# Kernel tuning notes

Hardware: AMD Instinct MI355X
Metric: run time of the kernel (lower is better)

Reference implementation:

```python
import jax, jax.numpy as jnp
import numpy as np


def _hilbert_filter(S):
    # scipy.signal.hilbert analytic-signal spectrum multiplier
    h = np.zeros(S, dtype=np.float32)
    h[0] = 1.0
    if S % 2 == 0:
        h[S // 2] = 1.0
        h[1:S // 2] = 2.0
    else:
        h[1:(S + 1) // 2] = 2.0
    return h


def setup_inputs() -> dict:
    key = jax.random.key(0)
    B, C, S = 16, 64, 2048
    x = jax.random.normal(key, (B, C, S), dtype=jnp.float32)
    return {"x": x}


def reference(x) -> jnp.ndarray:
    B, C, S = x.shape
    h = jnp.asarray(_hilbert_filter(S))
    # Analytic signal via FFT (batched over all B*C channels at once,
    # instead of recomputing hilbert() per (i,j) pair as the torch loop does)
    analytic = jnp.fft.ifft(jnp.fft.fft(x, axis=-1) * h, axis=-1)  # [B,C,S] complex
    theta = jnp.angle(analytic)                                    # [B,C,S]
    # Pairwise instantaneous phase differences: [B,C,C,S]
    d = theta[:, :, None, :] - theta[:, None, :, :]
    # angle(exp(1j*d)) wraps d to (-pi,pi]; original zeroes exact +/-pi values.
    # sign(sin(d)) == sign(wrapped d) with +/-pi (and 0) mapped to 0 -- identical math.
    pli = jnp.abs(jnp.mean(jnp.sign(jnp.sin(d)), axis=-1))         # [B,C,C]
    # diagonal: d == 0 -> sign 0 -> mean 0, matching the skipped i==j entries
    return pli.astype(jnp.float32)
```

## Files before the change

### kernel.cpp

```cpp
#include <hip/hip_runtime.h>

#define Bv 16
#define Cv 64
#define Sv 2048
#define NSEG 64
#define SSEG 32
#define ROWS 68

__device__ __forceinline__ void bf_f(float2& u, float2& v, const float2 w) {
    const float dr = u.x - v.x, di = u.y - v.y;
    u.x += v.x; u.y += v.y;
    v.x = dr * w.x - di * w.y;
    v.y = dr * w.y + di * w.x;
}
__device__ __forceinline__ void bf_i(float2& u, float2& v, const float2 w) {
    const float vr = v.x * w.x + v.y * w.y;
    const float vi = v.y * w.x - v.x * w.y;
    v.x = u.x - vr; v.y = u.y - vi;
    u.x += vr; u.y += vi;
}
__device__ __forceinline__ float2 csq(const float2 a) {
    return make_float2(a.x * a.x - a.y * a.y, 2.0f * a.x * a.y);
}
__device__ __forceinline__ float2 cm1(const float2 a) {
    const float cq = 0.70710678118654752f;
    return make_float2(cq * (a.x + a.y), cq * (a.y - a.x));
}
__device__ __forceinline__ float2 cmi(const float2 a) {
    return make_float2(a.y, -a.x);
}

__global__ __launch_bounds__(256) void hilbert_kernel(const float* __restrict__ x,
                                                      float* __restrict__ y) {
    __shared__ float2 zz[Sv];
    const int t = threadIdx.x;
    const int c0 = blockIdx.x * 2;
    const float* x0 = x + (size_t)c0 * Sv;
    const float* x1 = x0 + Sv;

    const float PI = 3.14159265358979323846f;
    float2 bA4, bB4, bC2;
    sincosf(-PI * (float)t * (1.0f / 1024.0f), &bA4.y, &bA4.x);
    sincosf(-PI * (float)(t & 31) * (1.0f / 128.0f), &bB4.y, &bB4.x);
    sincosf(-PI * (float)(t & 7) * (1.0f / 16.0f), &bC2.y, &bC2.x);
    const float2 bA2 = csq(bA4), bA1 = csq(bA2);
    const float2 bB2 = csq(bB4), bB1 = csq(bB2);
    const float2 bC1 = csq(bC2);

    float2 z[8];
    #pragma unroll
    for (int k = 0; k < 8; ++k)
        z[k] = make_float2(x0[t + 256 * k], x1[t + 256 * k]);

    {
        const float2 w1 = cm1(bA4);
        bf_f(z[0], z[4], bA4);      bf_f(z[1], z[5], w1);
        bf_f(z[2], z[6], cmi(bA4)); bf_f(z[3], z[7], cmi(w1));
        const float2 wB = cmi(bA2);
        bf_f(z[0], z[2], bA2); bf_f(z[1], z[3], wB);
        bf_f(z[4], z[6], bA2); bf_f(z[5], z[7], wB);
        bf_f(z[0], z[1], bA1); bf_f(z[2], z[3], bA1);
        bf_f(z[4], z[5], bA1); bf_f(z[6], z[7], bA1);
    }
    #pragma unroll
    for (int k = 0; k < 8; ++k) zz[t + 256 * k] = z[k];
    __syncthreads();

    {
        const int r = t & 31, base = (t >> 5) * 256 + r;
        #pragma unroll
        for (int k = 0; k < 8; ++k) z[k] = zz[base + 32 * k];
        const float2 w1 = cm1(bB4);
        bf_f(z[0], z[4], bB4);      bf_f(z[1], z[5], w1);
        bf_f(z[2], z[6], cmi(bB4)); bf_f(z[3], z[7], cmi(w1));
        const float2 wB = cmi(bB2);
        bf_f(z[0], z[2], bB2); bf_f(z[1], z[3], wB);
        bf_f(z[4], z[6], bB2); bf_f(z[5], z[7], wB);
        bf_f(z[0], z[1], bB1); bf_f(z[2], z[3], bB1);
        bf_f(z[4], z[5], bB1); bf_f(z[6], z[7], bB1);
        #pragma unroll
        for (int k = 0; k < 8; ++k) zz[base + 32 * k] = z[k];
    }
    __syncthreads();

    {
        const int r = t & 7, base0 = (t >> 3) * 32 + r, base1 = base0 + 1024;
        #pragma unroll
        for (int k = 0; k < 4; ++k) { z[k] = zz[base0 + 8 * k]; z[4 + k] = zz[base1 + 8 * k]; }
        const float2 wB = cmi(bC2);
        bf_f(z[0], z[2], bC2); bf_f(z[1], z[3], wB);
        bf_f(z[4], z[6], bC2); bf_f(z[5], z[7], wB);
        bf_f(z[0], z[1], bC1); bf_f(z[2], z[3], bC1);
        bf_f(z[4], z[5], bC1); bf_f(z[6], z[7], bC1);
        #pragma unroll
        for (int k = 0; k < 4; ++k) { zz[base0 + 8 * k] = z[k]; zz[base1 + 8 * k] = z[4 + k]; }
    }
    __syncthreads();

    {
        const int base = 8 * t;
        #pragma unroll
        for (int k = 0; k < 8; ++k) z[k] = zz[base + k];
        const float cq = 0.70710678118654752f;
        const float2 W1  = make_float2(1.0f, 0.0f);
        const float2 W41 = make_float2(cq, -cq);
        const float2 W42 = make_float2(0.0f, -1.0f);
        const float2 W43 = make_float2(-cq, -cq);
        bf_f(z[0], z[4], W1);  bf_f(z[1], z[5], W41);
        bf_f(z[2], z[6], W42); bf_f(z[3], z[7], W43);
        bf_f(z[0], z[2], W1); bf_f(z[1], z[3], W42);
        bf_f(z[4], z[6], W1); bf_f(z[5], z[7], W42);
        bf_f(z[0], z[1], W1); bf_f(z[2], z[3], W1);
        bf_f(z[4], z[5], W1); bf_f(z[6], z[7], W1);
        const float inv = 1.0f / (float)Sv;
        #pragma unroll
        for (int k = 0; k < 8; ++k) {
            const int kk = (int)(__brev((unsigned)(base + k)) >> 21);
            const float m = (kk == 0 || kk == Sv / 2) ? inv : (kk < Sv / 2 ? 2.0f * inv : 0.0f);
            z[k].x *= m; z[k].y *= m;
        }
        bf_i(z[0], z[1], W1); bf_i(z[2], z[3], W1);
        bf_i(z[4], z[5], W1); bf_i(z[6], z[7], W1);
        bf_i(z[0], z[2], W1); bf_i(z[1], z[3], W42);
        bf_i(z[4], z[6], W1); bf_i(z[5], z[7], W42);
        bf_i(z[0], z[4], W1);  bf_i(z[1], z[5], W41);
        bf_i(z[2], z[6], W42); bf_i(z[3], z[7], W43);
        #pragma unroll
        for (int k = 0; k < 8; ++k) zz[base + k] = z[k];
    }
    __syncthreads();

    {
        const int r = t & 7, base0 = (t >> 3) * 32 + r, base1 = base0 + 1024;
        #pragma unroll
        for (int k = 0; k < 4; ++k) { z[k] = zz[base0 + 8 * k]; z[4 + k] = zz[base1 + 8 * k]; }
        bf_i(z[0], z[1], bC1); bf_i(z[2], z[3], bC1);
        bf_i(z[4], z[5], bC1); bf_i(z[6], z[7], bC1);
        const float2 wB = cmi(bC2);
        bf_i(z[0], z[2], bC2); bf_i(z[1], z[3], wB);
        bf_i(z[4], z[6], bC2); bf_i(z[5], z[7], wB);
        #pragma unroll
        for (int k = 0; k < 4; ++k) { zz[base0 + 8 * k] = z[k]; zz[base1 + 8 * k] = z[4 + k]; }
    }
    __syncthreads();

    {
        const int r = t & 31, base = (t >> 5) * 256 + r;
        #pragma unroll
        for (int k = 0; k < 8; ++k) z[k] = zz[base + 32 * k];
        bf_i(z[0], z[1], bB1); bf_i(z[2], z[3], bB1);
        bf_i(z[4], z[5], bB1); bf_i(z[6], z[7], bB1);
        const float2 wB = cmi(bB2);
        bf_i(z[0], z[2], bB2); bf_i(z[1], z[3], wB);
        bf_i(z[4], z[6], bB2); bf_i(z[5], z[7], wB);
        const float2 w1 = cm1(bB4);
        bf_i(z[0], z[4], bB4);      bf_i(z[1], z[5], w1);
        bf_i(z[2], z[6], cmi(bB4)); bf_i(z[3], z[7], cmi(w1));
        #pragma unroll
        for (int k = 0; k < 8; ++k) zz[base + 32 * k] = z[k];
    }
    __syncthreads();

    {
        #pragma unroll
        for (int k = 0; k < 8; ++k) z[k] = zz[t + 256 * k];
        bf_i(z[0], z[1], bA1); bf_i(z[2], z[3], bA1);
        bf_i(z[4], z[5], bA1); bf_i(z[6], z[7], bA1);
        const float2 wB = cmi(bA2);
        bf_i(z[0], z[2], bA2); bf_i(z[1], z[3], wB);
        bf_i(z[4], z[6], bA2); bf_i(z[5], z[7], wB);
        const float2 w1 = cm1(bA4);
        bf_i(z[0], z[4], bA4);      bf_i(z[1], z[5], w1);
        bf_i(z[2], z[6], cmi(bA4)); bf_i(z[3], z[7], cmi(w1));
        float* y0 = y + (size_t)c0 * Sv;
        float* y1 = y0 + Sv;
        #pragma unroll
        for (int k = 0; k < 8; ++k) {
            const int n = t + 256 * k;
            y0[n] = z[k].y - x1[n];
            y1[n] = x0[n] - z[k].x;
        }
    }
}

__global__ __launch_bounds__(256) void pli_count_kernel(const float* __restrict__ x,
                                                        const float* __restrict__ y,
                                                        unsigned int* __restrict__ part) {
    __shared__ __align__(16) float xL[SSEG * ROWS];
    __shared__ __align__(16) float yL[SSEG * ROWS];
    const int blk = blockIdx.x;
    const int seg = blk & (NSEG - 1);
    const int b = blk >> 6;
    const int t = threadIdx.x;
    const float* xb = x + (size_t)b * Cv * Sv + seg * SSEG;
    const float* yb = y + (size_t)b * Cv * Sv + seg * SSEG;

    for (int e = t; e < Cv * SSEG; e += 256) {
        const int ch = e >> 5;
        const int s = e & (SSEG - 1);
        xL[s * ROWS + ch] = xb[(size_t)ch * Sv + s];
        yL[s * ROWS + ch] = yb[(size_t)ch * Sv + s];
    }
    __syncthreads();

    const int ti = t >> 4, tj = t & 15;
    const int i0 = ti * 4, j0 = tj * 4;
    int neg[4][4] = {};

    #pragma unroll 4
    for (int s = 0; s < SSEG; ++s) {
        const float4 xi = *(const float4*)&xL[s * ROWS + i0];
        const float4 yi = *(const float4*)&yL[s * ROWS + i0];
        const float4 xj = *(const float4*)&xL[s * ROWS + j0];
        const float4 yj = *(const float4*)&yL[s * ROWS + j0];
        const float xia[4] = {xi.x, xi.y, xi.z, xi.w};
        const float yia[4] = {yi.x, yi.y, yi.z, yi.w};
        const float xja[4] = {xj.x, xj.y, xj.z, xj.w};
        const float yja[4] = {yj.x, yj.y, yj.z, yj.w};
        #pragma unroll
        for (int a = 0; a < 4; ++a) {
            #pragma unroll
            for (int c = 0; c < 4; ++c) {
                const float cr = fmaf(yia[a], xja[c], -(xia[a] * yja[c]));
                neg[a][c] += (int)(__float_as_uint(cr) >> 31);
            }
        }
    }

    unsigned int* Pb = part + (size_t)(b * NSEG + seg) * (Cv * Cv / 4);
    #pragma unroll
    for (int a = 0; a < 4; ++a) {
        const unsigned int p = (unsigned)neg[a][0] | ((unsigned)neg[a][1] << 8)
                             | ((unsigned)neg[a][2] << 16) | ((unsigned)neg[a][3] << 24);
        Pb[(i0 + a) * (Cv / 4) + tj] = p;
    }
}

__global__ __launch_bounds__(256) void finalize_kernel(const unsigned int* __restrict__ part,
                                                       float* __restrict__ out) {
    const int idx = blockIdx.x * 256 + threadIdx.x;
    const int b = idx >> 12;
    const int ij = idx & 4095;
    const int i = ij >> 6, j = ij & 63;
    const unsigned int* p = part + (size_t)b * NSEG * 1024 + i * 16 + (j >> 2);
    const int sh = 8 * (j & 3);
    int negsum = 0;
    #pragma unroll 8
    for (int s = 0; s < NSEG; ++s)
        negsum += (int)((p[s * 1024] >> sh) & 0xFFu);
    out[idx] = (i == j) ? 0.0f
                        : fabsf((float)Sv - 2.0f * (float)negsum) * (1.0f / (float)Sv);
}

extern "C" void kernel_launch(void* const* d_in, const int* in_sizes, int n_in,
                              void* d_out, int out_size, void* d_ws, size_t ws_size,
                              hipStream_t stream) {
    const float* x = (const float*)d_in[0];
    float* y = (float*)d_ws;
    unsigned int* part = (unsigned int*)((char*)d_ws + (size_t)Bv * Cv * Sv * sizeof(float));
    float* out = (float*)d_out;

    hipLaunchKernelGGL(hilbert_kernel, dim3(Bv * Cv / 2), dim3(256), 0, stream, x, y);
    hipLaunchKernelGGL(pli_count_kernel, dim3(Bv * NSEG), dim3(256), 0, stream, x, y, part);
    hipLaunchKernelGGL(finalize_kernel, dim3(Bv * Cv * Cv / 256), dim3(256), 0, stream, part, out);
}
```

Baseline: 84.63 us.

## Exploit pairwise symmetry to compute only upper-triangle tile pairs

The count kernel now evaluates only 144 of the 256 4x4 channel-tile pairs, using cyclic offsets 0..8 so each unordered tile pair is covered once. It writes the packed counts contiguously as a uint4 per thread. The finalize kernel maps each (i,j) back to the stored tile, transposing within the tile when the offset exceeds 8, and reads the counts as bytes. This roughly halves the cross-product work and shrinks the partial-count buffer, but leaves 112 threads per block idle during compute and makes the finalize reads less regular.

Result: faster. 82.25 us (-2.8%).

```diff
diff --git a/kernel.cpp b/kernel.cpp
--- a/kernel.cpp
+++ b/kernel.cpp
@@ -6,6 +6,7 @@
 #define NSEG 64
 #define SSEG 32
 #define ROWS 68
+#define NTILE 144
 
 __device__ __forceinline__ void bf_f(float2& u, float2& v, const float2 w) {
     const float dr = u.x - v.x, di = u.y - v.y;
@@ -203,51 +204,60 @@
     }
     __syncthreads();
 
-    const int ti = t >> 4, tj = t & 15;
-    const int i0 = ti * 4, j0 = tj * 4;
-    int neg[4][4] = {};
-
-    #pragma unroll 4
-    for (int s = 0; s < SSEG; ++s) {
-        const float4 xi = *(const float4*)&xL[s * ROWS + i0];
-        const float4 yi = *(const float4*)&yL[s * ROWS + i0];
-        const float4 xj = *(const float4*)&xL[s * ROWS + j0];
-        const float4 yj = *(const float4*)&yL[s * ROWS + j0];
-        const float xia[4] = {xi.x, xi.y, xi.z, xi.w};
-        const float yia[4] = {yi.x, yi.y, yi.z, yi.w};
-        const float xja[4] = {xj.x, xj.y, xj.z, xj.w};
-        const float yja[4] = {yj.x, yj.y, yj.z, yj.w};
-        #pragma unroll
-        for (int a = 0; a < 4; ++a) {
+    if (t < NTILE) {
+        const int qi = t & 15;
+        const int dq = t >> 4;
+        const int i0 = qi * 4;
+        const int j0 = ((qi + dq) & 15) * 4;
+        int neg[4][4] = {};
+
+        #pragma unroll 4
+        for (int s = 0; s < SSEG; ++s) {
+            const float4 xi = *(const float4*)&xL[s * ROWS + i0];
+            const float4 yi = *(const float4*)&yL[s * ROWS + i0];
+            const float4 xj = *(const float4*)&xL[s * ROWS + j0];
+            const float4 yj = *(const float4*)&yL[s * ROWS + j0];
+            const float xia[4] = {xi.x, xi.y, xi.z, xi.w};
+            const float yia[4] = {yi.x, yi.y, yi.z, yi.w};
+            const float xja[4] = {xj.x, xj.y, xj.z, xj.w};
+            const float yja[4] = {yj.x, yj.y, yj.z, yj.w};
             #pragma unroll
-            for (int c = 0; c < 4; ++c) {
-                const float cr = fmaf(yia[a], xja[c], -(xia[a] * yja[c]));
-                neg[a][c] += (int)(__float_as_uint(cr) >> 31);
+            for (int a = 0; a < 4; ++a) {
+                #pragma unroll
+                for (int c = 0; c < 4; ++c) {
+                    const float cr = fmaf(yia[a], xja[c], -(xia[a] * yja[c]));
+                    neg[a][c] += (int)(__float_as_uint(cr) >> 31);
+                }
             }
         }
-    }
-
-    unsigned int* Pb = part + (size_t)(b * NSEG + seg) * (Cv * Cv / 4);
-    #pragma unroll
-    for (int a = 0; a < 4; ++a) {
-        const unsigned int p = (unsigned)neg[a][0] | ((unsigned)neg[a][1] << 8)
-                             | ((unsigned)neg[a][2] << 16) | ((unsigned)neg[a][3] << 24);
-        Pb[(i0 + a) * (Cv / 4) + tj] = p;
-    }
-}
-
-__global__ __launch_bounds__(256) void finalize_kernel(const unsigned int* __restrict__ part,
+
+        unsigned int* Pb = part + ((size_t)blk * NTILE + t) * 4;
+        unsigned int pk[4];
+        #pragma unroll
+        for (int a = 0; a < 4; ++a)
+            pk[a] = (unsigned)neg[a][0] | ((unsigned)neg[a][1] << 8)
+                  | ((unsigned)neg[a][2] << 16) | ((unsigned)neg[a][3] << 24);
+        *(uint4*)Pb = make_uint4(pk[0], pk[1], pk[2], pk[3]);
+    }
+}
+
+__global__ __launch_bounds__(256) void finalize_kernel(const unsigned char* __restrict__ part,
                                                        float* __restrict__ out) {
     const int idx = blockIdx.x * 256 + threadIdx.x;
     const int b = idx >> 12;
     const int ij = idx & 4095;
     const int i = ij >> 6, j = ij & 63;
-    const unsigned int* p = part + (size_t)b * NSEG * 1024 + i * 16 + (j >> 2);
-    const int sh = 8 * (j & 3);
+    const int qi = i >> 2, a = i & 3;
+    const int qj = j >> 2, c = j & 3;
+    const int g = (qj - qi) & 15;
+    int byteoff;
+    if (g <= 8) byteoff = (g * 16 + qi) * 16 + a * 4 + c;
+    else        byteoff = ((16 - g) * 16 + qj) * 16 + c * 4 + a;
+    const unsigned char* p = part + (size_t)b * NSEG * (NTILE * 16) + byteoff;
     int negsum = 0;
     #pragma unroll 8
     for (int s = 0; s < NSEG; ++s)
-        negsum += (int)((p[s * 1024] >> sh) & 0xFFu);
+        negsum += (int)p[s * (NTILE * 16)];
     out[idx] = (i == j) ? 0.0f
                         : fabsf((float)Sv - 2.0f * (float)negsum) * (1.0f / (float)Sv);
 }
@@ -262,5 +272,6 @@
 
     hipLaunchKernelGGL(hilbert_kernel, dim3(Bv * Cv / 2), dim3(256), 0, stream, x, y);
     hipLaunchKernelGGL(pli_count_kernel, dim3(Bv * NSEG), dim3(256), 0, stream, x, y, part);
-    hipLaunchKernelGGL(finalize_kernel, dim3(Bv * Cv * Cv / 256), dim3(256), 0, stream, part, out);
-}
+    hipLaunchKernelGGL(finalize_kernel, dim3(Bv * Cv * Cv / 256), dim3(256), 0, stream,
+                       (const unsigned char*)part, out);
+}
```
